# Optimization experiments

Measured on AMD Instinct MI355X. Metric: run time of the kernel, lower is better.

Reference implementation:

```python
import jax, jax.numpy as jnp
import numpy as np

N_NODES = 101001  # n_user + n_item + n_attr + 1
EMBED = 64
N_EDGES = 2020020  # ~avg degree 20
EPS = 1e-12


def setup_inputs() -> dict:
    key = jax.random.key(0)
    ks = jax.random.split(key, 8)
    h0 = jax.random.normal(ks[0], (N_NODES, EMBED), dtype=jnp.float32)
    h_att = jax.random.normal(ks[1], (N_NODES, EMBED), dtype=jnp.float32)
    t_att = jax.random.normal(ks[2], (N_NODES, EMBED), dtype=jnp.float32)
    w1 = jax.random.normal(ks[3], (EMBED, EMBED), dtype=jnp.float32) * (1.0 / np.sqrt(EMBED))
    b1 = jnp.zeros((EMBED,), dtype=jnp.float32)
    w2 = jax.random.normal(ks[4], (EMBED, EMBED), dtype=jnp.float32) * (1.0 / np.sqrt(EMBED))
    b2 = jnp.zeros((EMBED,), dtype=jnp.float32)
    edge_row = jnp.sort(jax.random.randint(ks[5], (N_EDGES,), 0, N_NODES, dtype=jnp.int32))
    edge_col = jax.random.randint(ks[6], (N_EDGES,), 0, N_NODES, dtype=jnp.int32)
    return {"h0": h0, "h_att": h_att, "t_att": t_att, "w1": w1, "b1": b1,
            "w2": w2, "b2": b2, "edge_row": edge_row, "edge_col": edge_col}


def _edge_softmax(h_att, t_att, edge_row, edge_col, n):
    # per-source-node softmax over ragged neighbor lists (kg_pair)
    logits = jnp.sum(h_att[edge_row] * t_att[edge_col], axis=-1)  # [E]
    m = jax.ops.segment_max(logits, edge_row, num_segments=n)
    e = jnp.exp(logits - m[edge_row])
    s = jax.ops.segment_sum(e, edge_row, num_segments=n)
    return e / jnp.maximum(s[edge_row], EPS)  # [E]


def reference(h0, h_att, t_att, w1, b1, w2, b2, edge_row, edge_col):
    n, d = h0.shape
    w = _edge_softmax(h_att, t_att, edge_row, edge_col, n)  # sparse attention weights
    h = h0
    all_embedding = [h0]
    for (W, b) in ((w1, b1), (w2, b2)):  # k = 1, 2 of ProP_n_Layer
        # n_embedding = SpMM(sp_weight, h)
        msg = jax.ops.segment_sum(w[:, None] * h[edge_col], edge_row, num_segments=n)
        add = h + msg
        h = jax.nn.relu(add @ W.T + b)
        norm = h / jnp.maximum(jnp.linalg.norm(h, axis=-1, keepdims=True), EPS)
        all_embedding.append(norm)
        h = norm  # normalized embedding feeds the next propagation layer
    return jnp.stack(all_embedding, axis=0)  # [n_layer, N, D]
```

## Files before the change

kernel.cpp:

```cpp
#include <hip/hip_runtime.h>
#include <math.h>

#define EMBED 64

__device__ __forceinline__ float dot4(float4 a, float4 b) {
    return fmaf(a.x, b.x, fmaf(a.y, b.y, fmaf(a.z, b.z, a.w * b.w)));
}

__device__ __forceinline__ float red16(float d) {
    d += __shfl_xor(d, 1);
    d += __shfl_xor(d, 2);
    d += __shfl_xor(d, 4);
    d += __shfl_xor(d, 8);
    return d;
}

__global__ void copy_h0_kernel(const float* __restrict__ h0, float* __restrict__ out, int n4) {
    int i = blockIdx.x * blockDim.x + threadIdx.x;
    if (i < n4) ((float4*)out)[i] = ((const float4*)h0)[i];
}

__global__ void build_rowptr_kernel(const int* __restrict__ row, int* __restrict__ rp, int E, int N) {
    int i = blockIdx.x * blockDim.x + threadIdx.x;
    if (i >= E) return;
    if (i == 0) {
        int r0 = row[0];
        for (int r = 0; r <= r0; ++r) rp[r] = 0;
    } else {
        int a = row[i - 1], b = row[i];
        for (int r = a + 1; r <= b; ++r) rp[r] = i;
    }
    if (i == E - 1) {
        int rl = row[E - 1];
        for (int r = rl + 1; r <= N; ++r) rp[r] = E;
    }
}

__global__ void __launch_bounds__(256, 8) logits_softmax_kernel(
        const float* __restrict__ ha, const float* __restrict__ ta,
        const int* __restrict__ col, const int* __restrict__ rp,
        float* __restrict__ ew, int N, int totalWaves) {
    __shared__ float lbuf[4][64];
    int wid = (blockIdx.x * blockDim.x + threadIdx.x) >> 6;
    int lane = threadIdx.x & 63;
    int wslot = threadIdx.x >> 6;
    int eg = lane >> 4, q = lane & 15;
    const float4* ta4 = (const float4*)ta;

    for (int n = wid; n < N; n += totalWaves) {
        int s = rp[n], t = rp[n + 1];
        int deg = t - s;
        if (deg <= 0) continue;
        float4 hv = ((const float4*)(ha + (size_t)n * EMBED))[q];

        if (deg <= 64) {
            int e0 = s;
            for (; e0 + 16 <= t; e0 += 16) {
                int i0 = e0 + eg, i1 = e0 + 4 + eg, i2 = e0 + 8 + eg, i3 = e0 + 12 + eg;
                int c0 = col[i0], c1 = col[i1], c2 = col[i2], c3 = col[i3];
                float4 v0 = ta4[(size_t)c0 * 16 + q];
                float4 v1 = ta4[(size_t)c1 * 16 + q];
                float4 v2 = ta4[(size_t)c2 * 16 + q];
                float4 v3 = ta4[(size_t)c3 * 16 + q];
                float d0 = red16(dot4(hv, v0));
                float d1 = red16(dot4(hv, v1));
                float d2 = red16(dot4(hv, v2));
                float d3 = red16(dot4(hv, v3));
                if (q == 0) {
                    lbuf[wslot][i0 - s] = d0; lbuf[wslot][i1 - s] = d1;
                    lbuf[wslot][i2 - s] = d2; lbuf[wslot][i3 - s] = d3;
                }
            }
            if (e0 < t) {
                int j0 = e0 + eg, j1 = e0 + 4 + eg, j2 = e0 + 8 + eg, j3 = e0 + 12 + eg;
                int i0 = min(j0, t - 1), i1 = min(j1, t - 1);
                int i2 = min(j2, t - 1), i3 = min(j3, t - 1);
                int c0 = col[i0], c1 = col[i1], c2 = col[i2], c3 = col[i3];
                float4 v0 = ta4[(size_t)c0 * 16 + q];
                float4 v1 = ta4[(size_t)c1 * 16 + q];
                float4 v2 = ta4[(size_t)c2 * 16 + q];
                float4 v3 = ta4[(size_t)c3 * 16 + q];
                float d0 = red16(dot4(hv, v0));
                float d1 = red16(dot4(hv, v1));
                float d2 = red16(dot4(hv, v2));
                float d3 = red16(dot4(hv, v3));
                if (q == 0) {
                    if (j0 < t) lbuf[wslot][j0 - s] = d0;
                    if (j1 < t) lbuf[wslot][j1 - s] = d1;
                    if (j2 < t) lbuf[wslot][j2 - s] = d2;
                    if (j3 < t) lbuf[wslot][j3 - s] = d3;
                }
            }
            asm volatile("s_waitcnt lgkmcnt(0)" ::: "memory");
            float v = (lane < deg) ? lbuf[wslot][lane] : -1e30f;
            float m = v;
            #pragma unroll
            for (int off = 32; off > 0; off >>= 1) m = fmaxf(m, __shfl_xor(m, off));
            float e = (lane < deg) ? __expf(v - m) : 0.f;
            float sum = e;
            #pragma unroll
            for (int off = 32; off > 0; off >>= 1) sum += __shfl_xor(sum, off);
            float inv = 1.f / fmaxf(sum, 1e-12f);
            if (lane < deg) ew[s + lane] = e * inv;
        } else {
            for (int e0 = s; e0 < t; e0 += 4) {
                int j0 = e0 + eg;
                int i0 = min(j0, t - 1);
                int c0 = col[i0];
                float4 v0 = ta4[(size_t)c0 * 16 + q];
                float d0 = red16(dot4(hv, v0));
                if (q == 0 && j0 < t) ew[j0] = d0;
            }
            asm volatile("s_waitcnt vmcnt(0)" ::: "memory");
            volatile const float* ewv = ew;
            float m = -1e30f;
            for (int e = s + lane; e < t; e += 64) m = fmaxf(m, ewv[e]);
            #pragma unroll
            for (int off = 32; off > 0; off >>= 1) m = fmaxf(m, __shfl_xor(m, off));
            float sum = 0.f;
            for (int e = s + lane; e < t; e += 64) sum += __expf(ewv[e] - m);
            #pragma unroll
            for (int off = 32; off > 0; off >>= 1) sum += __shfl_xor(sum, off);
            float inv = 1.f / fmaxf(sum, 1e-12f);
            for (int e = s + lane; e < t; e += 64) ew[e] = __expf(ewv[e] - m) * inv;
        }
    }
}

__global__ void __launch_bounds__(256, 8) spmm_kernel(
        const float* __restrict__ h_in, const int* __restrict__ col,
        const float* __restrict__ ew, const int* __restrict__ rp,
        float* __restrict__ add_out, int N, int totalWaves) {
    int wid = (blockIdx.x * blockDim.x + threadIdx.x) >> 6;
    int lane = threadIdx.x & 63;
    int eg = lane >> 4, q = lane & 15;
    const float4* h4 = (const float4*)h_in;

    for (int n = wid; n < N; n += totalWaves) {
        int s = rp[n], t = rp[n + 1];
        float4 self = h4[(size_t)n * 16 + q];
        float4 a0 = make_float4(0.f, 0.f, 0.f, 0.f);
        float4 a1 = make_float4(0.f, 0.f, 0.f, 0.f);
        int e0 = s;
        for (; e0 + 16 <= t; e0 += 16) {
            int i0 = e0 + eg, i1 = e0 + 4 + eg, i2 = e0 + 8 + eg, i3 = e0 + 12 + eg;
            int c0 = col[i0], c1 = col[i1], c2 = col[i2], c3 = col[i3];
            float w0 = ew[i0], w1 = ew[i1], w2 = ew[i2], w3 = ew[i3];
            float4 v0 = h4[(size_t)c0 * 16 + q];
            float4 v1 = h4[(size_t)c1 * 16 + q];
            float4 v2 = h4[(size_t)c2 * 16 + q];
            float4 v3 = h4[(size_t)c3 * 16 + q];
            a0.x = fmaf(w0, v0.x, a0.x); a0.y = fmaf(w0, v0.y, a0.y);
            a0.z = fmaf(w0, v0.z, a0.z); a0.w = fmaf(w0, v0.w, a0.w);
            a1.x = fmaf(w1, v1.x, a1.x); a1.y = fmaf(w1, v1.y, a1.y);
            a1.z = fmaf(w1, v1.z, a1.z); a1.w = fmaf(w1, v1.w, a1.w);
            a0.x = fmaf(w2, v2.x, a0.x); a0.y = fmaf(w2, v2.y, a0.y);
            a0.z = fmaf(w2, v2.z, a0.z); a0.w = fmaf(w2, v2.w, a0.w);
            a1.x = fmaf(w3, v3.x, a1.x); a1.y = fmaf(w3, v3.y, a1.y);
            a1.z = fmaf(w3, v3.z, a1.z); a1.w = fmaf(w3, v3.w, a1.w);
        }
        if (e0 < t) {
            int j0 = e0 + eg, j1 = e0 + 4 + eg, j2 = e0 + 8 + eg, j3 = e0 + 12 + eg;
            int i0 = min(j0, t - 1), i1 = min(j1, t - 1);
            int i2 = min(j2, t - 1), i3 = min(j3, t - 1);
            int c0 = col[i0], c1 = col[i1], c2 = col[i2], c3 = col[i3];
            float w0 = (j0 < t) ? ew[i0] : 0.f;
            float w1 = (j1 < t) ? ew[i1] : 0.f;
            float w2 = (j2 < t) ? ew[i2] : 0.f;
            float w3 = (j3 < t) ? ew[i3] : 0.f;
            float4 v0 = h4[(size_t)c0 * 16 + q];
            float4 v1 = h4[(size_t)c1 * 16 + q];
            float4 v2 = h4[(size_t)c2 * 16 + q];
            float4 v3 = h4[(size_t)c3 * 16 + q];
            a0.x = fmaf(w0, v0.x, a0.x); a0.y = fmaf(w0, v0.y, a0.y);
            a0.z = fmaf(w0, v0.z, a0.z); a0.w = fmaf(w0, v0.w, a0.w);
            a1.x = fmaf(w1, v1.x, a1.x); a1.y = fmaf(w1, v1.y, a1.y);
            a1.z = fmaf(w1, v1.z, a1.z); a1.w = fmaf(w1, v1.w, a1.w);
            a0.x = fmaf(w2, v2.x, a0.x); a0.y = fmaf(w2, v2.y, a0.y);
            a0.z = fmaf(w2, v2.z, a0.z); a0.w = fmaf(w2, v2.w, a0.w);
            a1.x = fmaf(w3, v3.x, a1.x); a1.y = fmaf(w3, v3.y, a1.y);
            a1.z = fmaf(w3, v3.z, a1.z); a1.w = fmaf(w3, v3.w, a1.w);
        }
        a0.x += a1.x; a0.y += a1.y; a0.z += a1.z; a0.w += a1.w;
        a0.x += __shfl_xor(a0.x, 16); a0.y += __shfl_xor(a0.y, 16);
        a0.z += __shfl_xor(a0.z, 16); a0.w += __shfl_xor(a0.w, 16);
        a0.x += __shfl_xor(a0.x, 32); a0.y += __shfl_xor(a0.y, 32);
        a0.z += __shfl_xor(a0.z, 32); a0.w += __shfl_xor(a0.w, 32);
        if (eg == 0) {
            float4 r;
            r.x = self.x + a0.x; r.y = self.y + a0.y;
            r.z = self.z + a0.z; r.w = self.w + a0.w;
            ((float4*)add_out)[(size_t)n * 16 + q] = r;
        }
    }
}

__global__ void __launch_bounds__(256, 4) dense_kernel(
        const float* __restrict__ W, const float* __restrict__ b,
        float* __restrict__ io, int N, int totalWaves) {
    __shared__ float4 rbuf[4][17];
    int wid = (blockIdx.x * blockDim.x + threadIdx.x) >> 6;
    int lane = threadIdx.x & 63;
    int ws = threadIdx.x >> 6;

    float4 Wr[16];
    const float4* W4 = (const float4*)W;
    #pragma unroll
    for (int p = 0; p < 16; ++p) Wr[p] = W4[lane * 16 + p];
    float bias = b[lane];
    float* rb = (float*)&rbuf[ws][0];

    float vcur = 0.f;
    if (wid < N) vcur = io[(size_t)wid * EMBED + lane];

    for (int n = wid; n < N; n += totalWaves) {
        rb[lane] = vcur;
        int n2 = n + totalWaves;
        float vnext = 0.f;
        if (n2 < N) vnext = io[(size_t)n2 * EMBED + lane];

        float x0 = bias, x1 = 0.f, x2 = 0.f, x3 = 0.f;
        #pragma unroll
        for (int j = 0; j < 4; ++j) {
            float4 a0 = rbuf[ws][4 * j + 0];
            float4 a1 = rbuf[ws][4 * j + 1];
            float4 a2 = rbuf[ws][4 * j + 2];
            float4 a3 = rbuf[ws][4 * j + 3];
            float4 w0 = Wr[4 * j + 0], w1 = Wr[4 * j + 1];
            float4 w2 = Wr[4 * j + 2], w3 = Wr[4 * j + 3];
            x0 = fmaf(a0.x, w0.x, x0); x0 = fmaf(a0.y, w0.y, x0);
            x0 = fmaf(a0.z, w0.z, x0); x0 = fmaf(a0.w, w0.w, x0);
            x1 = fmaf(a1.x, w1.x, x1); x1 = fmaf(a1.y, w1.y, x1);
            x1 = fmaf(a1.z, w1.z, x1); x1 = fmaf(a1.w, w1.w, x1);
            x2 = fmaf(a2.x, w2.x, x2); x2 = fmaf(a2.y, w2.y, x2);
            x2 = fmaf(a2.z, w2.z, x2); x2 = fmaf(a2.w, w2.w, x2);
            x3 = fmaf(a3.x, w3.x, x3); x3 = fmaf(a3.y, w3.y, x3);
            x3 = fmaf(a3.z, w3.z, x3); x3 = fmaf(a3.w, w3.w, x3);
        }
        float x = fmaxf((x0 + x1) + (x2 + x3), 0.f);

        float ss = x * x;
        #pragma unroll
        for (int off = 32; off > 0; off >>= 1) ss += __shfl_xor(ss, off);
        float scale = 1.f / fmaxf(sqrtf(ss), 1e-12f);
        io[(size_t)n * EMBED + lane] = x * scale;
        vcur = vnext;
    }
}

extern "C" void kernel_launch(void* const* d_in, const int* in_sizes, int n_in,
                              void* d_out, int out_size, void* d_ws, size_t ws_size,
                              hipStream_t stream) {
    const float* h0   = (const float*)d_in[0];
    const float* ha   = (const float*)d_in[1];
    const float* ta   = (const float*)d_in[2];
    const float* w1   = (const float*)d_in[3];
    const float* b1   = (const float*)d_in[4];
    const float* w2   = (const float*)d_in[5];
    const float* b2   = (const float*)d_in[6];
    const int*   erow = (const int*)d_in[7];
    const int*   ecol = (const int*)d_in[8];

    const int N = in_sizes[0] / EMBED;
    const int E = in_sizes[7];
    float* out = (float*)d_out;

    int*   rp = (int*)d_ws;
    size_t rp_bytes = ((size_t)(N + 1) * sizeof(int) + 255) & ~(size_t)255;
    float* ew = (float*)((char*)d_ws + rp_bytes);

    {
        int n4 = N * EMBED / 4;
        copy_h0_kernel<<<(n4 + 255) / 256, 256, 0, stream>>>(h0, out, n4);
    }
    build_rowptr_kernel<<<(E + 255) / 256, 256, 0, stream>>>(erow, rp, E, N);
    logits_softmax_kernel<<<2048, 256, 0, stream>>>(ha, ta, ecol, rp, ew, N, 2048 * 4);

    float* out1 = out + (size_t)N * EMBED;
    float* out2 = out + 2 * (size_t)N * EMBED;
    spmm_kernel<<<2048, 256, 0, stream>>>(h0, ecol, ew, rp, out1, N, 2048 * 4);
    dense_kernel<<<1024, 256, 0, stream>>>(w1, b1, out1, N, 1024 * 4);
    spmm_kernel<<<2048, 256, 0, stream>>>(out1, ecol, ew, rp, out2, N, 2048 * 4);
    dense_kernel<<<1024, 256, 0, stream>>>(w2, b2, out2, N, 1024 * 4);
}
```

Before: 441.8 us.

## Split fused node-wise logits+softmax into edge-parallel logits and node softmax kernels

Replaces the per-node fused kernel with an edge-parallel logits kernel that gathers both h_att[row] and t_att[col] per edge, followed by a separate per-node softmax kernel over the stored logits. This is meant to remove load imbalance from ragged degrees and the shared-memory staging. In exchange it re-gathers h_att rows per edge instead of once per node, adds a kernel launch, and makes an extra pass over the logits array.

```diff
diff --git a/kernel.cpp b/kernel.cpp
--- a/kernel.cpp
+++ b/kernel.cpp
@@ -36,94 +36,74 @@
     }
 }
 
-__global__ void __launch_bounds__(256, 8) logits_softmax_kernel(
+__global__ void __launch_bounds__(256, 8) edge_logits_kernel(
         const float* __restrict__ ha, const float* __restrict__ ta,
-        const int* __restrict__ col, const int* __restrict__ rp,
-        float* __restrict__ ew, int N, int totalWaves) {
-    __shared__ float lbuf[4][64];
+        const int* __restrict__ row, const int* __restrict__ col,
+        float* __restrict__ logits, int E, int totalWaves) {
     int wid = (blockIdx.x * blockDim.x + threadIdx.x) >> 6;
     int lane = threadIdx.x & 63;
-    int wslot = threadIdx.x >> 6;
     int eg = lane >> 4, q = lane & 15;
+    const float4* ha4 = (const float4*)ha;
     const float4* ta4 = (const float4*)ta;
 
-    for (int n = wid; n < N; n += totalWaves) {
-        int s = rp[n], t = rp[n + 1];
-        int deg = t - s;
-        if (deg <= 0) continue;
-        float4 hv = ((const float4*)(ha + (size_t)n * EMBED))[q];
-
-        if (deg <= 64) {
-            int e0 = s;
-            for (; e0 + 16 <= t; e0 += 16) {
-                int i0 = e0 + eg, i1 = e0 + 4 + eg, i2 = e0 + 8 + eg, i3 = e0 + 12 + eg;
-                int c0 = col[i0], c1 = col[i1], c2 = col[i2], c3 = col[i3];
-                float4 v0 = ta4[(size_t)c0 * 16 + q];
-                float4 v1 = ta4[(size_t)c1 * 16 + q];
-                float4 v2 = ta4[(size_t)c2 * 16 + q];
-                float4 v3 = ta4[(size_t)c3 * 16 + q];
-                float d0 = red16(dot4(hv, v0));
-                float d1 = red16(dot4(hv, v1));
-                float d2 = red16(dot4(hv, v2));
-                float d3 = red16(dot4(hv, v3));
-                if (q == 0) {
-                    lbuf[wslot][i0 - s] = d0; lbuf[wslot][i1 - s] = d1;
-                    lbuf[wslot][i2 - s] = d2; lbuf[wslot][i3 - s] = d3;
-                }
-            }
-            if (e0 < t) {
-                int j0 = e0 + eg, j1 = e0 + 4 + eg, j2 = e0 + 8 + eg, j3 = e0 + 12 + eg;
-                int i0 = min(j0, t - 1), i1 = min(j1, t - 1);
-                int i2 = min(j2, t - 1), i3 = min(j3, t - 1);
-                int c0 = col[i0], c1 = col[i1], c2 = col[i2], c3 = col[i3];
-                float4 v0 = ta4[(size_t)c0 * 16 + q];
-                float4 v1 = ta4[(size_t)c1 * 16 + q];
-                float4 v2 = ta4[(size_t)c2 * 16 + q];
-                float4 v3 = ta4[(size_t)c3 * 16 + q];
-                float d0 = red16(dot4(hv, v0));
-                float d1 = red16(dot4(hv, v1));
-                float d2 = red16(dot4(hv, v2));
-                float d3 = red16(dot4(hv, v3));
-                if (q == 0) {
-                    if (j0 < t) lbuf[wslot][j0 - s] = d0;
-                    if (j1 < t) lbuf[wslot][j1 - s] = d1;
-                    if (j2 < t) lbuf[wslot][j2 - s] = d2;
-                    if (j3 < t) lbuf[wslot][j3 - s] = d3;
-                }
-            }
-            asm volatile("s_waitcnt lgkmcnt(0)" ::: "memory");
-            float v = (lane < deg) ? lbuf[wslot][lane] : -1e30f;
-            float m = v;
-            #pragma unroll
-            for (int off = 32; off > 0; off >>= 1) m = fmaxf(m, __shfl_xor(m, off));
-            float e = (lane < deg) ? __expf(v - m) : 0.f;
-            float sum = e;
-            #pragma unroll
-            for (int off = 32; off > 0; off >>= 1) sum += __shfl_xor(sum, off);
-            float inv = 1.f / fmaxf(sum, 1e-12f);
-            if (lane < deg) ew[s + lane] = e * inv;
-        } else {
-            for (int e0 = s; e0 < t; e0 += 4) {
-                int j0 = e0 + eg;
-                int i0 = min(j0, t - 1);
-                int c0 = col[i0];
-                float4 v0 = ta4[(size_t)c0 * 16 + q];
-                float d0 = red16(dot4(hv, v0));
-                if (q == 0 && j0 < t) ew[j0] = d0;
-            }
-            asm volatile("s_waitcnt vmcnt(0)" ::: "memory");
-            volatile const float* ewv = ew;
-            float m = -1e30f;
-            for (int e = s + lane; e < t; e += 64) m = fmaxf(m, ewv[e]);
-            #pragma unroll
-            for (int off = 32; off > 0; off >>= 1) m = fmaxf(m, __shfl_xor(m, off));
-            float sum = 0.f;
-            for (int e = s + lane; e < t; e += 64) sum += __expf(ewv[e] - m);
-            #pragma unroll
-            for (int off = 32; off > 0; off >>= 1) sum += __shfl_xor(sum, off);
-            float inv = 1.f / fmaxf(sum, 1e-12f);
-            for (int e = s + lane; e < t; e += 64) ew[e] = __expf(ewv[e] - m) * inv;
-        }
+    for (int base = wid * 16; base < E; base += totalWaves * 16) {
+        int j0 = base + eg, j1 = base + 4 + eg, j2 = base + 8 + eg, j3 = base + 12 + eg;
+        int i0 = min(j0, E - 1), i1 = min(j1, E - 1);
+        int i2 = min(j2, E - 1), i3 = min(j3, E - 1);
+        int r0 = row[i0], r1 = row[i1], r2 = row[i2], r3 = row[i3];
+        int c0 = col[i0], c1 = col[i1], c2 = col[i2], c3 = col[i3];
+        float4 t0 = ta4[(size_t)c0 * 16 + q];
+        float4 t1 = ta4[(size_t)c1 * 16 + q];
+        float4 t2 = ta4[(size_t)c2 * 16 + q];
+        float4 t3 = ta4[(size_t)c3 * 16 + q];
+        float4 a0 = ha4[(size_t)r0 * 16 + q];
+        float4 a1 = ha4[(size_t)r1 * 16 + q];
+        float4 a2 = ha4[(size_t)r2 * 16 + q];
+        float4 a3 = ha4[(size_t)r3 * 16 + q];
+        float d0 = red16(dot4(a0, t0));
+        float d1 = red16(dot4(a1, t1));
+        float d2 = red16(dot4(a2, t2));
+        float d3 = red16(dot4(a3, t3));
+        if (q == 0) {
+            if (j0 < E) logits[j0] = d0;
+            if (j1 < E) logits[j1] = d1;
+            if (j2 < E) logits[j2] = d2;
+            if (j3 < E) logits[j3] = d3;
+        }
+    }
+}
+
+__global__ void __launch_bounds__(256) node_softmax_kernel(
+        const int* __restrict__ rp, float* __restrict__ lw, int N) {
+    int n = (blockIdx.x * blockDim.x + threadIdx.x) >> 6;
+    int lane = threadIdx.x & 63;
+    if (n >= N) return;
+    int s = rp[n], t = rp[n + 1];
+    int deg = t - s;
+    if (deg <= 0) return;
+
+    if (deg <= 64) {
+        float v = (lane < deg) ? lw[s + lane] : -1e30f;
+        float m = v;
+        #pragma unroll
+        for (int off = 32; off > 0; off >>= 1) m = fmaxf(m, __shfl_xor(m, off));
+        float e = (lane < deg) ? __expf(v - m) : 0.f;
+        float sum = e;
+        #pragma unroll
+        for (int off = 32; off > 0; off >>= 1) sum += __shfl_xor(sum, off);
+        float inv = 1.f / fmaxf(sum, 1e-12f);
+        if (lane < deg) lw[s + lane] = e * inv;
+    } else {
+        float m = -1e30f;
+        for (int e = s + lane; e < t; e += 64) m = fmaxf(m, lw[e]);
+        #pragma unroll
+        for (int off = 32; off > 0; off >>= 1) m = fmaxf(m, __shfl_xor(m, off));
+        float sum = 0.f;
+        for (int e = s + lane; e < t; e += 64) sum += __expf(lw[e] - m);
+        #pragma unroll
+        for (int off = 32; off > 0; off >>= 1) sum += __shfl_xor(sum, off);
+        float inv = 1.f / fmaxf(sum, 1e-12f);
+        for (int e = s + lane; e < t; e += 64) lw[e] = __expf(lw[e] - m) * inv;
     }
 }
 
@@ -274,7 +254,12 @@
         copy_h0_kernel<<<(n4 + 255) / 256, 256, 0, stream>>>(h0, out, n4);
     }
     build_rowptr_kernel<<<(E + 255) / 256, 256, 0, stream>>>(erow, rp, E, N);
-    logits_softmax_kernel<<<2048, 256, 0, stream>>>(ha, ta, ecol, rp, ew, N, 2048 * 4);
+    edge_logits_kernel<<<2048, 256, 0, stream>>>(ha, ta, erow, ecol, ew, E, 2048 * 4);
+    {
+        int waves_per_block = 256 / 64;
+        int blocks = (N + waves_per_block - 1) / waves_per_block;
+        node_softmax_kernel<<<blocks, 256, 0, stream>>>(rp, ew, N);
+    }
 
     float* out1 = out + (size_t)N * EMBED;
     float* out2 = out + 2 * (size_t)N * EMBED;
```

Result: slower. 462.1 us (+4.6%).
